# Kernel optimization log

Measured on AMD Instinct MI355X. Metric: run time of the kernel, lower is better.

The kernel has to match this reference:

```python
import jax, jax.numpy as jnp
import numpy as np

B, N, M = 2, 2048, 2048
DIM, CDIM = 1024, 1024
H, DH = 8, 64
INNER = H * DH
MULT = 8
SCALE = DH ** -0.5


def layer_norm(t, g, b, eps=1e-5):
    mu = t.mean(-1, keepdims=True)
    var = ((t - mu) ** 2).mean(-1, keepdims=True)
    return (t - mu) / jnp.sqrt(var + eps) * g + b


def setup_inputs() -> dict:
    key = jax.random.key(0)
    ks = jax.random.split(key, 24)
    w = lambda k, shape: (jax.random.normal(k, shape, dtype=jnp.float32) * 0.02)
    return {
        'x': jax.random.normal(ks[0], (B, N, DIM), dtype=jnp.float32),
        'context': jax.random.normal(ks[1], (B, M, CDIM), dtype=jnp.float32),
        'mask': jnp.ones((B, N), dtype=bool),
        'context_mask': jnp.ones((B, M), dtype=bool),
        'gx': jnp.ones((DIM,), jnp.float32), 'bx': jnp.zeros((DIM,), jnp.float32),
        'gc': jnp.ones((CDIM,), jnp.float32), 'bc': jnp.zeros((CDIM,), jnp.float32),
        'w_qk': w(ks[2], (DIM, INNER)), 'w_cqk': w(ks[3], (CDIM, INNER)),
        'w_v': w(ks[4], (DIM, INNER)), 'w_cv': w(ks[5], (CDIM, INNER)),
        'w_out': w(ks[6], (INNER, DIM)), 'b_out': jnp.zeros((DIM,), jnp.float32),
        'w_cout': w(ks[7], (INNER, CDIM)), 'b_cout': jnp.zeros((CDIM,), jnp.float32),
        'w_th': w(ks[8], (H, H)), 'w_cth': w(ks[9], (H, H)),
        'ffg': jnp.ones((DIM,), jnp.float32), 'ffb': jnp.zeros((DIM,), jnp.float32),
        'ffw1': w(ks[10], (DIM, MULT * DIM)), 'ffb1': jnp.zeros((MULT * DIM,), jnp.float32),
        'ffw2': w(ks[11], (MULT * DIM, DIM)), 'ffb2': jnp.zeros((DIM,), jnp.float32),
        'cffg': jnp.ones((CDIM,), jnp.float32), 'cffb': jnp.zeros((CDIM,), jnp.float32),
        'cffw1': w(ks[12], (CDIM, MULT * CDIM)), 'cffb1': jnp.zeros((MULT * CDIM,), jnp.float32),
        'cffw2': w(ks[13], (MULT * CDIM, CDIM)), 'cffb2': jnp.zeros((CDIM,), jnp.float32),
    }


def reference(x, context, mask, context_mask, gx, bx, gc, bc,
              w_qk, w_cqk, w_v, w_cv, w_out, b_out, w_cout, b_cout,
              w_th, w_cth, ffg, ffb, ffw1, ffb1, ffw2, ffb2,
              cffg, cffb, cffw1, cffb1, cffw2, cffb2):
    xn = layer_norm(x, gx, bx)
    cn = layer_norm(context, gc, bc)
    split = lambda t: t.reshape(t.shape[0], t.shape[1], H, DH).transpose(0, 2, 1, 3)  # b n (h d) -> b h n d
    qk, v = split(xn @ w_qk), split(xn @ w_v)
    cqk, cv = split(cn @ w_cqk), split(cn @ w_cv)
    sim = jnp.einsum('bhid,bhjd->bhij', qk, cqk) * SCALE
    attn_mask = mask[:, None, :, None] & context_mask[:, None, None, :]
    sim = jnp.where(attn_mask, sim, -jnp.finfo(sim.dtype).max)
    attn = jax.nn.softmax(sim, axis=-1)        # x attends over context (j)
    cattn = jax.nn.softmax(sim, axis=-2)       # context attends over x (i)
    attn = jnp.einsum('bhij,gh->bgij', attn, w_th)       # talking heads (1x1 conv over head dim)
    cattn = jnp.einsum('bhij,gh->bgij', cattn, w_cth)
    out = jnp.einsum('bhij,bhjd->bhid', attn, cv).transpose(0, 2, 1, 3).reshape(x.shape[0], -1, INNER)
    cout = jnp.einsum('bhij,bhid->bhjd', cattn, v).transpose(0, 2, 1, 3).reshape(context.shape[0], -1, INNER)
    x = x + out @ w_out + b_out
    context = context + cout @ w_cout + b_cout
    x = x + (jax.nn.gelu(layer_norm(x, ffg, ffb) @ ffw1 + ffb1, approximate=False) @ ffw2 + ffb2)
    context = context + (jax.nn.gelu(layer_norm(context, cffg, cffb) @ cffw1 + cffb1, approximate=False) @ cffw2 + cffb2)
    return x, context
```

## Files before the change

kernel.cpp:

```cpp
#include <hip/hip_runtime.h>
#include <hip/hip_bf16.h>
#include <math.h>

#define BB 2
#define NN 2048
#define MM 2048
#define DIMD 1024
#define HH 8
#define DHD 64
#define INNERD 512
#define FFD 8192
#define SCALE_QK 0.125f
#define LOG2E 1.44269504088896f

typedef __hip_bfloat16 bf16;
typedef float f32x4 __attribute__((ext_vector_type(4)));
typedef short short8 __attribute__((ext_vector_type(8)));
static const long long NM = (long long)NN * MM;

__device__ __forceinline__ float cvt(float v) { return v; }
__device__ __forceinline__ float cvt(bf16 v) { return __bfloat162float(v); }
__device__ __forceinline__ void stc(float* p, float v) { *p = v; }
__device__ __forceinline__ void stc(bf16* p, float v) { *p = __float2bfloat16(v); }

__device__ __forceinline__ float bits2f(short u) {
    return __uint_as_float(((unsigned)(unsigned short)u) << 16);
}
__device__ __forceinline__ short bf16bits(float f) {
    bf16 t = __float2bfloat16(f);
    short s;
    __builtin_memcpy(&s, &t, 2);
    return s;
}

__device__ __forceinline__ void gl_lds16(const bf16* g, bf16* l) {
    __builtin_amdgcn_global_load_lds(
        (const __attribute__((address_space(1))) void*)(g),
        (__attribute__((address_space(3))) void*)(l), 16, 0, 0);
}

__device__ __forceinline__ float block_reduce_sum(float v) {
    __shared__ float sh[4];
    int tid = threadIdx.x;
#pragma unroll
    for (int off = 32; off > 0; off >>= 1) v += __shfl_down(v, off, 64);
    __syncthreads();
    if ((tid & 63) == 0) sh[tid >> 6] = v;
    __syncthreads();
    return sh[0] + sh[1] + sh[2] + sh[3];
}

__global__ __launch_bounds__(256) void layernorm_k(const float* __restrict__ in,
                                                   bf16* __restrict__ out,
                                                   const float* __restrict__ g,
                                                   const float* __restrict__ b) {
    long long row = blockIdx.x;
    const float* xr = in + row * DIMD;
    bf16* yr = out + row * DIMD;
    int tid = threadIdx.x;
    float s = 0.f;
    for (int i = tid; i < DIMD; i += 256) s += xr[i];
    float mean = block_reduce_sum(s) * (1.0f / DIMD);
    float s2 = 0.f;
    for (int i = tid; i < DIMD; i += 256) { float d = xr[i] - mean; s2 += d * d; }
    float var = block_reduce_sum(s2) * (1.0f / DIMD);
    float inv = 1.0f / sqrtf(var + 1e-5f);
    for (int i = tid; i < DIMD; i += 256)
        yr[i] = __float2bfloat16((xr[i] - mean) * inv * g[i] + b[i]);
}

__global__ __launch_bounds__(256) void biasadd_k(float* __restrict__ out,
                                                 const float* __restrict__ bias) {
    long long idx = (long long)blockIdx.x * 256 + threadIdx.x;
    f32x4 v = ((f32x4*)out)[idx];
    const f32x4 bv = ((const f32x4*)bias)[idx & (DIMD / 4 - 1)];
    v.x += bv.x; v.y += bv.y; v.z += bv.z; v.w += bv.w;
    ((f32x4*)out)[idx] = v;
}

template <typename TI>
__global__ __launch_bounds__(256) void transpose_k(const TI* __restrict__ in,
                                                   bf16* __restrict__ out,
                                                   int R, int C) {
    __shared__ bf16 t[32][33];
    int bc = blockIdx.x * 32, br = blockIdx.y * 32;
    int tid = threadIdx.x;
    int c = tid & 31, r0 = tid >> 5;
#pragma unroll
    for (int s = 0; s < 4; s++) {
        int r = r0 + s * 8;
        t[r][c] = __float2bfloat16(cvt(in[(long long)(br + r) * C + bc + c]));
    }
    __syncthreads();
#pragma unroll
    for (int s = 0; s < 4; s++) {
        int r = r0 + s * 8;
        out[(long long)(bc + r) * R + br + c] = t[c][r];
    }
}

__global__ __launch_bounds__(256) void colstats_part_k(const bf16* __restrict__ sim,
                                                       float* __restrict__ mcp,
                                                       float* __restrict__ lcp) {
    int j = blockIdx.x * 256 + threadIdx.x;
    int h = blockIdx.y;
    int ic = blockIdx.z;
    const bf16* base = sim + (long long)h * NM + (long long)ic * 128 * MM + j;
    float m = -3.4e38f;
#pragma unroll 8
    for (int i = 0; i < 128; i++) m = fmaxf(m, cvt(base[(long long)i * MM]));
    float s = 0.f;
#pragma unroll 8
    for (int i = 0; i < 128; i++)
        s += exp2f((cvt(base[(long long)i * MM]) - m) * LOG2E);
    mcp[((long long)ic * HH + h) * MM + j] = m;
    lcp[((long long)ic * HH + h) * MM + j] = s;
}

__global__ __launch_bounds__(256) void colstats_comb_k(const float* __restrict__ mcp,
                                                       const float* __restrict__ lcp,
                                                       float* __restrict__ mc,
                                                       float* __restrict__ lc) {
    int idx = blockIdx.x * 256 + threadIdx.x;
    int h = idx >> 11, j = idx & (MM - 1);
    float m = -3.4e38f;
#pragma unroll
    for (int ic = 0; ic < 16; ic++) m = fmaxf(m, mcp[((long long)ic * HH + h) * MM + j]);
    float l = 0.f;
#pragma unroll
    for (int ic = 0; ic < 16; ic++)
        l += lcp[((long long)ic * HH + h) * MM + j] *
             exp2f((mcp[((long long)ic * HH + h) * MM + j] - m) * LOG2E);
    mc[idx] = m;
    lc[idx] = l;
}

__global__ __launch_bounds__(256) void mixcolT_k(const bf16* __restrict__ sim,
                                                 bf16* __restrict__ simT,
                                                 const float* __restrict__ w,
                                                 const float* __restrict__ mc,
                                                 const float* __restrict__ lc) {
    __shared__ __align__(16) bf16 t[HH * 64 * 32];
    __shared__ float ws_[64];
    int j0 = blockIdx.x * 32, i0 = blockIdx.y * 64;
    int tid = threadIdx.x;
    if (tid < 64) ws_[tid] = w[tid];
#pragma unroll
    for (int q = 0; q < 8; q++) {
        int c = q * 256 + tid;
        int h = c >> 8, r = (c >> 2) & 63, jc = c & 3;
        short8 x = *(const short8*)&sim[(long long)h * NM + (long long)(i0 + r) * MM + j0 + jc * 8];
        *(short8*)&t[h * 2048 + r * 32 + (jc ^ ((r >> 3) & 3)) * 8] = x;
    }
    __syncthreads();
    int jl = tid >> 3, io = tid & 7;
    int jg = j0 + jl;
    float e[HH][8];
#pragma unroll
    for (int h = 0; h < HH; h++) {
        float mcj = mc[h * MM + jg];
        float rl = 1.0f / lc[h * MM + jg];
#pragma unroll
        for (int k = 0; k < 8; k++) {
            int il = io * 8 + k;
            float v = cvt(t[h * 2048 + il * 32 + (((jl >> 3) ^ io) & 3) * 8 + (jl & 7)]);
            e[h][k] = exp2f((v - mcj) * LOG2E) * rl;
        }
    }
#pragma unroll
    for (int g = 0; g < HH; g++) {
        short8 o;
#pragma unroll
        for (int k = 0; k < 8; k++) {
            float acc = 0.f;
#pragma unroll
            for (int h = 0; h < HH; h++) acc += ws_[g * 8 + h] * e[h][k];
            o[k] = bf16bits(acc);
        }
        *(short8*)&simT[(long long)g * NM + (long long)jg * MM + i0 + io * 8] = o;
    }
}

__global__ __launch_bounds__(256) void rowsoftmix_k(bf16* __restrict__ sim,
                                                    const float* __restrict__ w) {
    __shared__ float ws_[64];
    __shared__ float redm[HH][4];
    __shared__ float redl[HH][4];
    long long i = blockIdx.x;
    int tid = threadIdx.x, lane = tid & 63, wv = tid >> 6;
    if (tid < 64) ws_[tid] = w[tid];
    bf16* rowbase = sim + i * MM + tid * 8;
    float v[HH][8];
#pragma unroll
    for (int h = 0; h < HH; h++) {
        short8 r = *(const short8*)(rowbase + (long long)h * NM);
#pragma unroll
        for (int c = 0; c < 8; c++) v[h][c] = bits2f(r[c]);
    }
    float mh[HH];
#pragma unroll
    for (int h = 0; h < HH; h++) {
        float m = fmaxf(fmaxf(fmaxf(v[h][0], v[h][1]), fmaxf(v[h][2], v[h][3])),
                        fmaxf(fmaxf(v[h][4], v[h][5]), fmaxf(v[h][6], v[h][7])));
#pragma unroll
        for (int off = 32; off > 0; off >>= 1) m = fmaxf(m, __shfl_xor(m, off, 64));
        if (lane == 0) redm[h][wv] = m;
    }
    __syncthreads();
#pragma unroll
    for (int h = 0; h < HH; h++)
        mh[h] = fmaxf(fmaxf(redm[h][0], redm[h][1]), fmaxf(redm[h][2], redm[h][3]));
#pragma unroll
    for (int h = 0; h < HH; h++) {
        float s = 0.f;
#pragma unroll
        for (int c = 0; c < 8; c++) {
            v[h][c] = exp2f((v[h][c] - mh[h]) * LOG2E);
            s += v[h][c];
        }
#pragma unroll
        for (int off = 32; off > 0; off >>= 1) s += __shfl_xor(s, off, 64);
        if (lane == 0) redl[h][wv] = s;
    }
    __syncthreads();
#pragma unroll
    for (int h = 0; h < HH; h++) {
        float inv = 1.0f / (redl[h][0] + redl[h][1] + redl[h][2] + redl[h][3]);
#pragma unroll
        for (int c = 0; c < 8; c++) v[h][c] *= inv;
    }
#pragma unroll
    for (int g = 0; g < HH; g++) {
        short8 o;
#pragma unroll
        for (int c = 0; c < 8; c++) {
            float acc = 0.f;
#pragma unroll
            for (int h = 0; h < HH; h++) acc += ws_[g * 8 + h] * v[h][c];
            o[c] = bf16bits(acc);
        }
        *(short8*)(rowbase + (long long)g * NM) = o;
    }
}

template <int BM, int BN, int WROWS, int ZMODE, bool ATOMIC, typename CT>
__global__ __launch_bounds__(256) void mgemm(
    const bf16* __restrict__ A, const bf16* __restrict__ B, CT* __restrict__ C,
    int K, int lda, int ldb, int ldc,
    long long sA, long long sB, long long sC,
    float alpha, const float* __restrict__ bias, const float* __restrict__ bias2,
    const float* __restrict__ residual, const float* __restrict__ residual2,
    int ldr, int gelu_flag) {
    constexpr int BK = 32;
    constexpr int WCOLS = 4 / WROWS;
    constexpr int WM = BM / WROWS, WN = BN / WCOLS;
    constexpr int FM = WM / 16, FN = WN / 16;
    constexpr int ACH = BM * BK / 8;
    constexpr int BCH = BN * BK / 8;
    __shared__ bf16 As[BM * BK];
    __shared__ bf16 Bs[BN * BK];
    int z = blockIdx.z;
    int m0 = blockIdx.y * BM, n0 = blockIdx.x * BN;
    if (ZMODE == 0) A += z * sA;
    else if (ZMODE == 1) A += (long long)(z >> 1) * sA;
    else if (ZMODE == 2) A += ((long long)(((m0 >> 11) << 1) + z) * 2048 - m0) * lda;
    B += z * sB;
    C += z * sC;
    const float* bb_ = bias;
    const float* rr_ = residual;
    if (ZMODE == 2 && z) { bb_ = bias2; rr_ = residual2; }
    int tid = threadIdx.x, lane = tid & 63, w = tid >> 6;
    int wm = (w / WCOLS) * WM, wn = (w % WCOLS) * WN;
    f32x4 acc[FM][FN] = {};
    for (int k0 = 0; k0 < K; k0 += BK) {
        __syncthreads();
#pragma unroll
        for (int c = tid; c < ACH; c += 256) {
            int row = c >> 2, col = (c & 3) * 8;
            gl_lds16(A + (long long)(m0 + row) * lda + k0 + col, As + c * 8);
        }
#pragma unroll
        for (int c = tid; c < BCH; c += 256) {
            int row = c >> 2, col = (c & 3) * 8;
            gl_lds16(B + (long long)(n0 + row) * ldb + k0 + col, Bs + c * 8);
        }
        __syncthreads();
        short8 af[FM], bfr[FN];
#pragma unroll
        for (int fm = 0; fm < FM; fm++)
            af[fm] = *(const short8*)&As[(wm + fm * 16 + (lane & 15)) * BK + (lane >> 4) * 8];
#pragma unroll
        for (int fn = 0; fn < FN; fn++)
            bfr[fn] = *(const short8*)&Bs[(wn + fn * 16 + (lane & 15)) * BK + (lane >> 4) * 8];
#pragma unroll
        for (int fm = 0; fm < FM; fm++)
#pragma unroll
            for (int fn = 0; fn < FN; fn++)
                acc[fm][fn] = __builtin_amdgcn_mfma_f32_16x16x32_bf16(af[fm], bfr[fn], acc[fm][fn], 0, 0, 0);
    }
#pragma unroll
    for (int fm = 0; fm < FM; fm++) {
#pragma unroll
        for (int fn = 0; fn < FN; fn++) {
#pragma unroll
            for (int r = 0; r < 4; r++) {
                int m = m0 + wm + fm * 16 + (lane >> 4) * 4 + r;
                int n = n0 + wn + fn * 16 + (lane & 15);
                float v = acc[fm][fn][r] * alpha;
                if (bb_) v += bb_[n];
                if (rr_) v += rr_[(long long)m * ldr + n];
                if (gelu_flag) v = 0.5f * v * (1.0f + erff(v * 0.70710678118654752440f));
                if (ATOMIC) atomicAdd((float*)&C[(long long)m * ldc + n], v);
                else stc(&C[(long long)m * ldc + n], v);
            }
        }
    }
}

template <bool GELU, bool ATOMIC, typename CT>
__global__ __launch_bounds__(512, 2) void mgemm256(
    const bf16* __restrict__ A, const bf16* __restrict__ B, CT* __restrict__ C,
    int K, int lda, int ldb, int ldc,
    long long sA, long long sB, long long sC,
    const float* __restrict__ bias) {
    __shared__ bf16 sm[65536];
    const int T = K >> 6;
    int z = blockIdx.z;
    A += (long long)z * sA;
    B += (long long)z * sB;
    C += (long long)z * sC;
    int gx = gridDim.x;
    int nwg = gx * gridDim.y;
    int id = blockIdx.y * gx + blockIdx.x;
    id = (id & 7) * (nwg >> 3) + (id >> 3);
    int n0 = (id % gx) * 256;
    int m0 = (id / gx) * 256;

    int tid = threadIdx.x, lane = tid & 63, w = tid >> 6;
    int wrow = w >> 2, wcol = w & 3;
    int sr = tid >> 3;
    int ecol = (((tid >> 3) ^ tid) & 7) * 8;

    auto stage = [&](const bf16* g, int ld, int row0, int k0, bf16* l) {
        const bf16* s = g + (long long)(row0 + sr) * ld + k0 + ecol;
        gl_lds16(s, l + (tid << 3));
        gl_lds16(s + (long long)(ld << 6), l + 4096 + (tid << 3));
    };

    f32x4 acc[8][4] = {};

    stage(A, lda, m0, 0, sm);
    stage(A, lda, m0 + 128, 0, sm + 8192);
    stage(B, ldb, n0, 0, sm + 32768);
    stage(B, ldb, n0 + 128, 0, sm + 32768 + 8192);
    if (T > 1) {
        stage(B, ldb, n0, 64, sm + 32768 + 16384);
        stage(B, ldb, n0 + 128, 64, sm + 32768 + 16384 + 8192);
        asm volatile("s_waitcnt vmcnt(4)" ::: "memory");
    } else {
        asm volatile("s_waitcnt vmcnt(0)" ::: "memory");
    }
    __builtin_amdgcn_s_barrier();

    for (int kt = 0; kt < T; ++kt) {
        const int cur = kt & 1, nxt = cur ^ 1;
        const bf16* Ab = sm + cur * 16384;
        const bf16* Bb = sm + 32768 + cur * 16384;
        short8 bf_[4][2];
#pragma unroll
        for (int fn = 0; fn < 4; fn++)
#pragma unroll
            for (int kk = 0; kk < 2; kk++) {
                int row = wcol * 64 + fn * 16 + (lane & 15);
                int cb = (kk * 64 + ((lane >> 4) << 4)) ^ ((row & 7) << 4);
                bf_[fn][kk] = *(const short8*)((const char*)Bb + row * 128 + cb);
            }
#pragma unroll
        for (int q = 0; q < 4; q++) {
            short8 af[2][2];
#pragma unroll
            for (int i = 0; i < 2; i++)
#pragma unroll
                for (int kk = 0; kk < 2; kk++) {
                    int row = wrow * 128 + (q * 2 + i) * 16 + (lane & 15);
                    int cb = (kk * 64 + ((lane >> 4) << 4)) ^ ((row & 7) << 4);
                    af[i][kk] = *(const short8*)((const char*)Ab + row * 128 + cb);
                }
            if (q == 0) {
                if (kt + 1 < T) stage(A, lda, m0, (kt + 1) << 6, sm + nxt * 16384);
            } else if (q == 1) {
                if (kt + 1 < T) stage(A, lda, m0 + 128, (kt + 1) << 6, sm + nxt * 16384 + 8192);
            } else if (q == 2) {
                if (kt + 2 < T) stage(B, ldb, n0, (kt + 2) << 6, sm + 32768 + cur * 16384);
            } else {
                if (kt + 2 < T) {
                    stage(B, ldb, n0 + 128, (kt + 2) << 6, sm + 32768 + cur * 16384 + 8192);
                    asm volatile("s_waitcnt vmcnt(4)" ::: "memory");
                } else {
                    asm volatile("s_waitcnt vmcnt(0)" ::: "memory");
                }
            }
            __builtin_amdgcn_s_barrier();
            __builtin_amdgcn_s_setprio(1);
#pragma unroll
            for (int i = 0; i < 2; i++)
#pragma unroll
                for (int fn = 0; fn < 4; fn++)
#pragma unroll
                    for (int kk = 0; kk < 2; kk++)
                        acc[q * 2 + i][fn] = __builtin_amdgcn_mfma_f32_16x16x32_bf16(
                            af[i][kk], bf_[fn][kk], acc[q * 2 + i][fn], 0, 0, 0);
            __builtin_amdgcn_s_setprio(0);
            __builtin_amdgcn_s_barrier();
        }
    }

    long long crow0 = m0 + wrow * 128 + ((lane >> 4) << 2);
    int ccol0 = n0 + wcol * 64 + (lane & 15);
#pragma unroll
    for (int fm = 0; fm < 8; fm++)
#pragma unroll
        for (int fn = 0; fn < 4; fn++)
#pragma unroll
            for (int r = 0; r < 4; r++) {
                long long m = crow0 + fm * 16 + r;
                int n = ccol0 + fn * 16;
                float v = acc[fm][fn][r];
                if (bias) v += bias[n];
                if (GELU) v = 0.5f * v * (1.0f + erff(v * 0.70710678118654752440f));
                if (ATOMIC) atomicAdd((float*)&C[m * ldc + n], v);
                else stc(&C[m * ldc + n], v);
            }
}

__global__ __launch_bounds__(256) void pv_k(const bf16* __restrict__ P,
                                            const bf16* __restrict__ Vt,
                                            bf16* __restrict__ O) {
    constexpr int BK = 32;
    __shared__ bf16 As[64 * BK];
    __shared__ bf16 Bs[64 * BK];
    int z = blockIdx.z;
    int h = z & 7, sel = z >> 3;
    const bf16* A = P + (long long)z * NM;
    const bf16* B = Vt + (long long)z * DHD * NN;
    bf16* C = O + (long long)sel * NN * INNERD + h * DHD;
    int m0 = blockIdx.y * 64;
    int tid = threadIdx.x, lane = tid & 63, w = tid >> 6;
    int wm = w * 16;
    f32x4 acc[4] = {};
    for (int k0 = 0; k0 < NN; k0 += BK) {
        __syncthreads();
        {
            int row = tid >> 2, col = (tid & 3) * 8;
            gl_lds16(A + (long long)(m0 + row) * MM + k0 + col, As + tid * 8);
            gl_lds16(B + (long long)row * NN + k0 + col, Bs + tid * 8);
        }
        __syncthreads();
        short8 af = *(const short8*)&As[(wm + (lane & 15)) * BK + (lane >> 4) * 8];
#pragma unroll
        for (int fn = 0; fn < 4; fn++) {
            short8 bfr = *(const short8*)&Bs[(fn * 16 + (lane & 15)) * BK + (lane >> 4) * 8];
            acc[fn] = __builtin_amdgcn_mfma_f32_16x16x32_bf16(af, bfr, acc[fn], 0, 0, 0);
        }
    }
#pragma unroll
    for (int fn = 0; fn < 4; fn++)
#pragma unroll
        for (int r = 0; r < 4; r++) {
            int m = m0 + wm + (lane >> 4) * 4 + r;
            int n = fn * 16 + (lane & 15);
            stc(&C[(long long)m * INNERD + n], acc[fn][r]);
        }
}

extern "C" void kernel_launch(void* const* d_in, const int* in_sizes, int n_in,
                              void* d_out, int out_size, void* d_ws, size_t ws_size,
                              hipStream_t stream) {
    const float* x = (const float*)d_in[0];
    const float* context = (const float*)d_in[1];
    const float* gx = (const float*)d_in[4];
    const float* bx = (const float*)d_in[5];
    const float* gc = (const float*)d_in[6];
    const float* bc = (const float*)d_in[7];
    const float* w_qk = (const float*)d_in[8];
    const float* w_cqk = (const float*)d_in[9];
    const float* w_v = (const float*)d_in[10];
    const float* w_cv = (const float*)d_in[11];
    const float* w_out = (const float*)d_in[12];
    const float* b_out = (const float*)d_in[13];
    const float* w_cout = (const float*)d_in[14];
    const float* b_cout = (const float*)d_in[15];
    const float* w_th = (const float*)d_in[16];
    const float* w_cth = (const float*)d_in[17];
    const float* ffg = (const float*)d_in[18];
    const float* ffb = (const float*)d_in[19];
    const float* ffw1 = (const float*)d_in[20];
    const float* ffb1 = (const float*)d_in[21];
    const float* ffw2 = (const float*)d_in[22];
    const float* ffb2 = (const float*)d_in[23];
    const float* cffg = (const float*)d_in[24];
    const float* cffb = (const float*)d_in[25];
    const float* cffw1 = (const float*)d_in[26];
    const float* cffb1 = (const float*)d_in[27];
    const float* cffw2 = (const float*)d_in[28];
    const float* cffb2 = (const float*)d_in[29];

    const long long TOK = (long long)BB * NN;

    bf16* xn = (bf16*)d_ws;
    bf16* cn = xn + TOK * DIMD;
    bf16* qk = cn + TOK * DIMD;
    bf16* vv = qk + TOK * INNERD;
    bf16* cqk = vv + TOK * INNERD;
    bf16* cv = cqk + TOK * INNERD;
    bf16* outb = cv + TOK * INNERD;
    bf16* sim = outb + (long long)BB * 2 * NN * INNERD;
    bf16* w4 = sim + (long long)HH * NM;
    bf16* ffw1T = w4;
    bf16* cffw1T = ffw1T + (long long)FFD * DIMD;
    bf16* ffw2T = cffw1T + (long long)FFD * DIMD;
    bf16* cffw2T = ffw2T + (long long)DIMD * FFD;
    bf16* simT = w4;
    bf16* wqkT = w4 + 4LL * FFD * DIMD;
    bf16* wvT = wqkT + (long long)INNERD * DIMD;
    bf16* wcqkT = wvT + (long long)INNERD * DIMD;
    bf16* wcvT = wcqkT + (long long)INNERD * DIMD;
    bf16* woutT = wcvT + (long long)INNERD * DIMD;
    bf16* wcoutT = woutT + (long long)DIMD * INNERD;
    bf16* cvT = wcoutT + (long long)DIMD * INNERD;
    bf16* vT = cvT + (long long)INNERD * NN;
    float* stats = (float*)(vT + (long long)INNERD * NN);
    float* mc = stats;
    float* lc = mc + HH * MM;
    float* mcp = lc + HH * MM;
    float* lcp = mcp + 16 * HH * MM;

    float* out_x = (float*)d_out;
    float* out_c = out_x + TOK * DIMD;

    dim3 blk(256);

    transpose_k<float><<<dim3(INNERD / 32, DIMD / 32), blk, 0, stream>>>(w_qk, wqkT, DIMD, INNERD);
    transpose_k<float><<<dim3(INNERD / 32, DIMD / 32), blk, 0, stream>>>(w_v, wvT, DIMD, INNERD);
    transpose_k<float><<<dim3(INNERD / 32, DIMD / 32), blk, 0, stream>>>(w_cqk, wcqkT, DIMD, INNERD);
    transpose_k<float><<<dim3(INNERD / 32, DIMD / 32), blk, 0, stream>>>(w_cv, wcvT, DIMD, INNERD);
    transpose_k<float><<<dim3(DIMD / 32, INNERD / 32), blk, 0, stream>>>(w_out, woutT, INNERD, DIMD);
    transpose_k<float><<<dim3(DIMD / 32, INNERD / 32), blk, 0, stream>>>(w_cout, wcoutT, INNERD, DIMD);

    layernorm_k<<<TOK, blk, 0, stream>>>(x, xn, gx, bx);
    layernorm_k<<<TOK, blk, 0, stream>>>(context, cn, gc, bc);

    {
        dim3 g(INNERD / 128, TOK / 128, 4);
        mgemm<128, 128, 2, 1, false, bf16><<<g, blk, 0, stream>>>(xn, wqkT, qk,
            DIMD, DIMD, DIMD, INNERD,
            TOK * DIMD, (long long)INNERD * DIMD, TOK * INNERD,
            1.f, nullptr, nullptr, nullptr, nullptr, 0, 0);
    }

    for (int b = 0; b < BB; b++) {
        const bf16* qk_b = qk + (long long)b * NN * INNERD;
        const bf16* cqk_b = cqk + (long long)b * NN * INNERD;
        const bf16* v_b = vv + (long long)b * NN * INNERD;
        const bf16* cv_b = cv + (long long)b * NN * INNERD;
        bf16* outb_b = outb + (long long)b * 2 * NN * INNERD;

        transpose_k<bf16><<<dim3(INNERD / 32, NN / 32), blk, 0, stream>>>(cv_b, cvT, NN, INNERD);
        transpose_k<bf16><<<dim3(INNERD / 32, NN / 32), blk, 0, stream>>>(v_b, vT, NN, INNERD);

        {
            dim3 gs(MM / 128, NN / 128, HH);
            mgemm<128, 128, 2, 0, false, bf16><<<gs, blk, 0, stream>>>(qk_b, cqk_b, sim,
                DHD, INNERD, INNERD, MM, DHD, DHD, NM,
                SCALE_QK, nullptr, nullptr, nullptr, nullptr, 0, 0);
        }
        {
            dim3 g(MM / 256, HH, 16);
            colstats_part_k<<<g, blk, 0, stream>>>(sim, mcp, lcp);
        }
        colstats_comb_k<<<HH * MM / 256, blk, 0, stream>>>(mcp, lcp, mc, lc);
        mixcolT_k<<<dim3(MM / 32, NN / 64), blk, 0, stream>>>(sim, simT, w_cth, mc, lc);
        rowsoftmix_k<<<NN, blk, 0, stream>>>(sim, w_th);
        pv_k<<<dim3(1, NN / 64, 16), blk, 0, stream>>>(sim, cvT, outb_b);
    }

    {
        dim3 g(DIMD / 128, TOK / 128, 2);
        mgemm<128, 128, 2, 2, false, float><<<g, blk, 0, stream>>>(outb, woutT, out_x,
            INNERD, INNERD, INNERD, DIMD,
            0, (long long)DIMD * INNERD, TOK * DIMD,
            1.f, b_out, b_cout, x, context, DIMD, 0);
    }

    transpose_k<float><<<dim3(FFD / 32, DIMD / 32), blk, 0, stream>>>(ffw1, ffw1T, DIMD, FFD);
    transpose_k<float><<<dim3(FFD / 32, DIMD / 32), blk, 0, stream>>>(cffw1, cffw1T, DIMD, FFD);
    transpose_k<float><<<dim3(DIMD / 32, FFD / 32), blk, 0, stream>>>(ffw2, ffw2T, FFD, DIMD);
    transpose_k<float><<<dim3(DIMD / 32, FFD / 32), blk, 0, stream>>>(cffw2, cffw2T, FFD, DIMD);

    const float* g_[2] = {ffg, cffg};
    const float* bterm_[2] = {ffb, cffb};
    const float* b1_[2] = {ffb1, cffb1};
    const float* b2_[2] = {ffb2, cffb2};
    const bf16* w1T_[2] = {ffw1T, cffw1T};
    const bf16* w2T_[2] = {ffw2T, cffw2T};
    float* outp_[2] = {out_x, out_c};
    bf16* lnb = xn;
    bf16* hid = sim;
    for (int m = 0; m < 2; m++) {
        layernorm_k<<<TOK, blk, 0, stream>>>(outp_[m], lnb, g_[m], bterm_[m]);
        biasadd_k<<<TOK * DIMD / 1024, blk, 0, stream>>>(outp_[m], b2_[m]);
        {
            dim3 g(FFD / 256, TOK / 256, 1);
            mgemm256<true, false, bf16><<<g, dim3(512), 0, stream>>>(lnb, w1T_[m], hid,
                DIMD, DIMD, DIMD, FFD, 0, 0, 0, b1_[m]);
        }
        {
            dim3 g(DIMD / 256, TOK / 256, 4);
            mgemm256<false, true, float><<<g, dim3(512), 0, stream>>>(hid, w2T_[m], outp_[m],
                FFD / 4, FFD, FFD, DIMD, 2048, 2048, 0, nullptr);
        }
    }
}
```

Before: 1.196 ms.

## Replace atomic split-K FFN down-projection with 2-way split plus merge; faster GELU

```diff
diff --git a/kernel.cpp b/kernel.cpp
--- a/kernel.cpp
+++ b/kernel.cpp
@@ -31,6 +31,18 @@
     short s;
     __builtin_memcpy(&s, &t, 2);
     return s;
+}
+
+__device__ __forceinline__ float gelu_f(float v) {
+    float z = fabsf(v) * 0.70710678118654752440f;
+    float t = __builtin_amdgcn_rcpf(__builtin_fmaf(0.3275911f, z, 1.0f));
+    float inner = __builtin_fmaf(
+        t, __builtin_fmaf(t, __builtin_fmaf(t, __builtin_fmaf(t, 1.061405429f, -1.453152027f),
+                                            1.421413741f), -0.284496736f), 0.254829592f);
+    float p = t * inner;
+    float e = exp2f(-z * z * LOG2E);
+    float erfz = __builtin_fmaf(-p, e, 1.0f);
+    return 0.5f * v * (1.0f + copysignf(erfz, v));
 }
 
 __device__ __forceinline__ void gl_lds16(const bf16* g, bf16* l) {
@@ -76,6 +88,15 @@
     const f32x4 bv = ((const f32x4*)bias)[idx & (DIMD / 4 - 1)];
     v.x += bv.x; v.y += bv.y; v.z += bv.z; v.w += bv.w;
     ((f32x4*)out)[idx] = v;
+}
+
+__global__ __launch_bounds__(256) void addmerge_k(float* __restrict__ out,
+                                                  const float* __restrict__ pp) {
+    long long idx = (long long)blockIdx.x * 256 + threadIdx.x;
+    f32x4 a = ((f32x4*)out)[idx];
+    f32x4 b = ((const f32x4*)pp)[idx];
+    a.x += b.x; a.y += b.y; a.z += b.z; a.w += b.w;
+    ((f32x4*)out)[idx] = a;
 }
 
 template <typename TI>
@@ -309,7 +330,7 @@
                 float v = acc[fm][fn][r] * alpha;
                 if (bb_) v += bb_[n];
                 if (rr_) v += rr_[(long long)m * ldr + n];
-                if (gelu_flag) v = 0.5f * v * (1.0f + erff(v * 0.70710678118654752440f));
+                if (gelu_flag) v = gelu_f(v);
                 if (ATOMIC) atomicAdd((float*)&C[(long long)m * ldc + n], v);
                 else stc(&C[(long long)m * ldc + n], v);
             }
@@ -317,9 +338,10 @@
     }
 }
 
-template <bool GELU, bool ATOMIC, typename CT>
+template <bool GELU, int CMODE, typename CT>
 __global__ __launch_bounds__(512, 2) void mgemm256(
     const bf16* __restrict__ A, const bf16* __restrict__ B, CT* __restrict__ C,
+    CT* __restrict__ C2,
     int K, int lda, int ldb, int ldc,
     long long sA, long long sB, long long sC,
     const float* __restrict__ bias) {
@@ -417,6 +439,11 @@
 
     long long crow0 = m0 + wrow * 128 + ((lane >> 4) << 2);
     int ccol0 = n0 + wcol * 64 + (lane & 15);
+    float bcol[4] = {0.f, 0.f, 0.f, 0.f};
+    if (bias) {
+#pragma unroll
+        for (int fn = 0; fn < 4; fn++) bcol[fn] = bias[ccol0 + fn * 16];
+    }
 #pragma unroll
     for (int fm = 0; fm < 8; fm++)
 #pragma unroll
@@ -425,11 +452,17 @@
             for (int r = 0; r < 4; r++) {
                 long long m = crow0 + fm * 16 + r;
                 int n = ccol0 + fn * 16;
-                float v = acc[fm][fn][r];
-                if (bias) v += bias[n];
-                if (GELU) v = 0.5f * v * (1.0f + erff(v * 0.70710678118654752440f));
-                if (ATOMIC) atomicAdd((float*)&C[m * ldc + n], v);
-                else stc(&C[m * ldc + n], v);
+                float v = acc[fm][fn][r] + bcol[fn];
+                if (GELU) v = gelu_f(v);
+                if (CMODE == 1) {
+                    if (z == 0) {
+                        C[m * ldc + n] += v;
+                    } else {
+                        stc(&C2[m * ldc + n], v);
+                    }
+                } else {
+                    stc(&C[m * ldc + n], v);
+                }
             }
 }
 
@@ -534,6 +567,7 @@
     float* lc = mc + HH * MM;
     float* mcp = lc + HH * MM;
     float* lcp = mcp + 16 * HH * MM;
+    float* pp = (float*)qk;
 
     float* out_x = (float*)d_out;
     float* out_c = out_x + TOK * DIMD;
@@ -611,13 +645,14 @@
         biasadd_k<<<TOK * DIMD / 1024, blk, 0, stream>>>(outp_[m], b2_[m]);
         {
             dim3 g(FFD / 256, TOK / 256, 1);
-            mgemm256<true, false, bf16><<<g, dim3(512), 0, stream>>>(lnb, w1T_[m], hid,
-                DIMD, DIMD, DIMD, FFD, 0, 0, 0, b1_[m]);
+            mgemm256<true, 0, bf16><<<g, dim3(512), 0, stream>>>(lnb, w1T_[m], hid,
+                (bf16*)nullptr, DIMD, DIMD, DIMD, FFD, 0, 0, 0, b1_[m]);
         }
         {
-            dim3 g(DIMD / 256, TOK / 256, 4);
-            mgemm256<false, true, float><<<g, dim3(512), 0, stream>>>(hid, w2T_[m], outp_[m],
-                FFD / 4, FFD, FFD, DIMD, 2048, 2048, 0, nullptr);
-        }
-    }
-}
+            dim3 g(DIMD / 256, TOK / 256, 2);
+            mgemm256<false, 1, float><<<g, dim3(512), 0, stream>>>(hid, w2T_[m], outp_[m],
+                pp, FFD / 2, FFD, FFD, DIMD, 4096, 4096, 0, nullptr);
+        }
+        addmerge_k<<<TOK * DIMD / 1024, blk, 0, stream>>>(outp_[m], pp);
+    }
+}
```

Result: no change. 1.182 ms (-1.1%).
